# Performance work log

Measured on AMD Instinct MI355X. Metric: run time of the kernel, lower is better.

The kernel has to match this reference:

```python
import jax, jax.numpy as jnp
import numpy as np

EPS = 1e-6
H, KV, HD, FF = 16, 8, 128, 3072

def rmsnorm(x, scale):
    # qwen3_compatible: compute in fp32, scale, cast back
    xf = x.astype(jnp.float32)
    var = jnp.mean(xf * xf, axis=-1, keepdims=True)
    return ((xf * jax.lax.rsqrt(var + EPS)) * scale).astype(x.dtype)

def apply_rope(x, cos, sin):
    # x: [b, h, s, d]; cos/sin: [s, d]
    d = x.shape[-1]
    x1, x2 = x[..., : d // 2], x[..., d // 2 :]
    rotated = jnp.concatenate([-x2, x1], axis=-1)
    return (x * cos[None, None] + rotated * sin[None, None]).astype(x.dtype)

def setup_inputs() -> dict:
    key = jax.random.key(0)
    B, S, D = 2, 2048, 1024
    ks = jax.random.split(key, 8)
    x = jax.random.normal(ks[0], (B, S, D), jnp.float32)
    mask = jnp.triu(jnp.ones((S, S), dtype=bool), k=1)  # True = masked (causal)
    # Qwen3 RoPE, base 1e6, full-dim cos/sin (halves duplicated)
    pos = jnp.arange(S, dtype=jnp.float32)
    inv_freq = 1.0 / (1e6 ** (jnp.arange(0, HD, 2, dtype=jnp.float32) / HD))
    ang = pos[:, None] * inv_freq[None, :]
    cos = jnp.concatenate([jnp.cos(ang), jnp.cos(ang)], axis=-1)
    sin = jnp.concatenate([jnp.sin(ang), jnp.sin(ang)], axis=-1)
    s = 0.02
    wq = jax.random.normal(ks[1], (D, H * HD), jnp.float32) * s
    wk = jax.random.normal(ks[2], (D, KV * HD), jnp.float32) * s
    wv = jax.random.normal(ks[3], (D, KV * HD), jnp.float32) * s
    wo = jax.random.normal(ks[4], (H * HD, D), jnp.float32) * s
    fc1 = jax.random.normal(ks[5], (D, FF), jnp.float32) * s
    fc2 = jax.random.normal(ks[6], (D, FF), jnp.float32) * s
    fc3 = jax.random.normal(ks[7], (FF, D), jnp.float32) * s
    return dict(x=x, mask=mask, cos=cos, sin=sin, wq=wq, wk=wk, wv=wv, wo=wo,
                fc1=fc1, fc2=fc2, fc3=fc3,
                norm1_scale=jnp.ones((D,), jnp.float32),
                norm2_scale=jnp.ones((D,), jnp.float32),
                q_norm_scale=jnp.ones((HD,), jnp.float32),
                k_norm_scale=jnp.ones((HD,), jnp.float32))

def reference(x, mask, cos, sin, wq, wk, wv, wo, fc1, fc2, fc3,
              norm1_scale, norm2_scale, q_norm_scale, k_norm_scale):
    B, S, D = x.shape
    G = H // KV  # GQA group size
    # --- attention sublayer ---
    h = rmsnorm(x, norm1_scale)
    q = (h @ wq).reshape(B, S, H, HD).transpose(0, 2, 1, 3)   # [b,h,s,d]
    k = (h @ wk).reshape(B, S, KV, HD).transpose(0, 2, 1, 3)  # [b,kv,s,d]
    v = (h @ wv).reshape(B, S, KV, HD).transpose(0, 2, 1, 3)
    q = rmsnorm(q, q_norm_scale)
    k = rmsnorm(k, k_norm_scale)
    q = apply_rope(q, cos, sin)
    k = apply_rope(k, cos, sin)
    k = jnp.repeat(k, G, axis=1)  # repeat_interleave over head dim
    v = jnp.repeat(v, G, axis=1)
    scores = jnp.einsum('bhqd,bhkd->bhqk', q, k)
    scores = jnp.where(mask[None, None], -jnp.inf, scores)
    w = jax.nn.softmax(scores / np.float32(np.sqrt(HD)), axis=-1)
    ctx = jnp.einsum('bhqk,bhkd->bqhd', w, v).reshape(B, S, H * HD)
    x = x + ctx @ wo
    # --- SwiGLU FFN sublayer ---
    h2 = rmsnorm(x, norm2_scale)
    ff = (jax.nn.silu(h2 @ fc1) * (h2 @ fc2)) @ fc3
    return x + ff
```

## Files before the change

kernel.cpp:

```cpp
#include <hip/hip_runtime.h>

#define B_  2
#define S_  2048
#define D_  1024
#define H_  16
#define KV_ 8
#define HD_ 128
#define FF_ 3072
#define KVB 32

typedef short bf16x8 __attribute__((ext_vector_type(8)));
typedef short bf16x4 __attribute__((ext_vector_type(4)));
typedef float f32x4 __attribute__((ext_vector_type(4)));

__device__ __forceinline__ float bf2f(unsigned short u) {
    union { float f; unsigned int i; } c; c.i = ((unsigned int)u) << 16; return c.f;
}
__device__ __forceinline__ unsigned short f2bf(float f) {
    union { float f; unsigned int i; } c; c.f = f;
    unsigned int r = c.i + 0x7fffu + ((c.i >> 16) & 1u);
    return (unsigned short)(r >> 16);
}
__device__ __forceinline__ unsigned int cvtpk_bf16(float lo, float hi) {
    unsigned int r;
    asm("v_cvt_pk_bf16_f32 %0, %1, %2" : "=v"(r) : "v"(lo), "v"(hi));
    return r;
}

__device__ __forceinline__ void gload_lds16(const unsigned short* g, char* ldsbase) {
    __builtin_amdgcn_global_load_lds(
        (const __attribute__((address_space(1))) unsigned int*)g,
        (__attribute__((address_space(3))) unsigned int*)ldsbase, 16, 0, 0);
}

__device__ __forceinline__ f32x4 pv_mfma(bf16x4 a, bf16x4 b, f32x4 c) {
#if __has_builtin(__builtin_amdgcn_mfma_f32_16x16x16bf16_1k)
    return __builtin_amdgcn_mfma_f32_16x16x16bf16_1k(a, b, c, 0, 0, 0);
#elif __has_builtin(__builtin_amdgcn_mfma_f32_16x16x16_bf16)
    return __builtin_amdgcn_mfma_f32_16x16x16_bf16(a, b, c, 0, 0, 0);
#else
    f32x4 d;
    asm("v_mfma_f32_16x16x16_bf16 %0, %1, %2, %3" : "=v"(d) : "v"(a), "v"(b), "v"(c));
    return d;
#endif
}

__global__ __launch_bounds__(256)
void rmsnorm_kernel(const float* __restrict__ in, const float* __restrict__ scale,
                    unsigned short* __restrict__ out) {
    const int row = blockIdx.x;
    const int t = threadIdx.x;
    const float4 v = *reinterpret_cast<const float4*>(in + (size_t)row * D_ + t * 4);
    float s = v.x * v.x + v.y * v.y + v.z * v.z + v.w * v.w;
    #pragma unroll
    for (int o = 32; o; o >>= 1) s += __shfl_down(s, o);
    __shared__ float red[4];
    const int lane = t & 63, wid = t >> 6;
    if (lane == 0) red[wid] = s;
    __syncthreads();
    s = red[0] + red[1] + red[2] + red[3];
    const float rn = rsqrtf(s * (1.0f / D_) + 1e-6f);
    const float4 sc = *reinterpret_cast<const float4*>(scale + t * 4);
    unsigned short o4[4];
    o4[0] = f2bf(v.x * rn * sc.x);
    o4[1] = f2bf(v.y * rn * sc.y);
    o4[2] = f2bf(v.z * rn * sc.z);
    o4[3] = f2bf(v.w * rn * sc.w);
    *reinterpret_cast<ushort4*>(out + (size_t)row * D_ + t * 4) =
        *reinterpret_cast<ushort4*>(o4);
}

struct WTDesc {
    const float* src[7];
    unsigned short* dst[7];
    int K[7];
    int N[7];
    int start[8];
};

__global__ __launch_bounds__(256)
void wtrans_all_kernel(WTDesc d) {
    __shared__ float tile[32][33];
    const int blk = blockIdx.x;
    int i = 0;
    #pragma unroll
    for (int j = 0; j < 7; ++j) if (blk >= d.start[j + 1]) i = j + 1;
    const int local = blk - d.start[i];
    const int K = d.K[i], N = d.N[i];
    const int nkt = K >> 5;
    const int kt = (local % nkt) * 32, nt = (local / nkt) * 32;
    const float* W = d.src[i];
    unsigned short* Wt = d.dst[i];
    const int t = threadIdx.x;
    {
        const int r = t >> 3, c4 = (t & 7) * 4;
        const float4 v = *reinterpret_cast<const float4*>(W + (size_t)(kt + r) * N + nt + c4);
        tile[r][c4] = v.x; tile[r][c4 + 1] = v.y; tile[r][c4 + 2] = v.z; tile[r][c4 + 3] = v.w;
    }
    __syncthreads();
    {
        const int n = t >> 3, k4 = (t & 7) * 4;
        unsigned short o[4];
        #pragma unroll
        for (int q = 0; q < 4; q++) o[q] = f2bf(tile[k4 + q][n]);
        *reinterpret_cast<ushort4*>(Wt + (size_t)(nt + n) * K + kt + k4) =
            *reinterpret_cast<ushort4*>(o);
    }
}

__global__ __launch_bounds__(256)
void vtrans_kernel(const unsigned short* __restrict__ vin, unsigned short* __restrict__ vt) {
    __shared__ unsigned short tile[32][36];
    const int t = threadIdx.x;
    const int mt = blockIdx.x * 32, nt = blockIdx.y * 32;
    {
        const int r = t >> 3, c4 = (t & 7) * 4;
        *reinterpret_cast<ushort4*>(&tile[r][c4]) =
            *reinterpret_cast<const ushort4*>(vin + (size_t)(mt + r) * 4096 + nt + c4);
    }
    __syncthreads();
    {
        const int n = t >> 3, m4 = (t & 7) * 4;
        unsigned short o[4];
        #pragma unroll
        for (int q = 0; q < 4; q++) o[q] = tile[m4 + q][n];
        *reinterpret_cast<ushort4*>(vt + (size_t)(nt + n) * 4096 + mt + m4) =
            *reinterpret_cast<ushort4*>(o);
    }
}

__global__ __launch_bounds__(512, 2)
void gemm256(const unsigned short* __restrict__ A, const unsigned short* __restrict__ Bt,
             unsigned short* __restrict__ C, int M, int N, int K, int nm) {
    __shared__ __align__(16) char lds[131072];
    const int tid = threadIdx.x;
    const int lane = tid & 63, w = tid >> 6;
    const int lm = lane & 15, lg = lane >> 4;
    const int wr = w >> 2, wc = w & 3;
    const int nwg = gridDim.x;
    const int cpx = nwg >> 3;
    const int bid = blockIdx.x;
    const int swz = (bid & 7) * cpx + (bid >> 3);
    const int m0 = (swz % nm) * 256;
    const int n0 = (swz / nm) * 256;

    f32x4 acc[8][4];
    #pragma unroll
    for (int i = 0; i < 8; ++i)
        #pragma unroll
        for (int j = 0; j < 4; ++j) acc[i][j] = (f32x4){0.f, 0.f, 0.f, 0.f};

    const int srow = tid >> 3;
    const int skel = ((tid & 7) * 8) ^ (((tid >> 5) & 1) << 4);
    const int flip = ((lm >> 2) & 1) << 5;
    const int abase = (wr * 128 + lm) * 128 + ((lg * 16) ^ flip);
    const int bbase = (wc * 64 + lm) * 128 + ((lg * 16) ^ flip);

    auto part1 = [&](int kt, int d) {
        const unsigned short* ga = A + (size_t)(m0 + srow) * K + kt * 64 + skel;
        const unsigned short* gb = Bt + (size_t)(n0 + srow) * K + kt * 64 + skel;
        char* la = lds + d * 65536 + (w << 10);
        char* lb = la + 32768;
        gload_lds16(gb,                      lb);
        gload_lds16(gb + (size_t)64 * K,     lb + 8192);
        gload_lds16(gb + (size_t)128 * K,    lb + 16384);
        gload_lds16(gb + (size_t)192 * K,    lb + 24576);
        gload_lds16(ga,                      la);
        gload_lds16(ga + (size_t)128 * K,    la + 16384);
    };
    auto part2 = [&](int kt, int d) {
        const unsigned short* ga = A + (size_t)(m0 + srow) * K + kt * 64 + skel;
        char* la = lds + d * 65536 + (w << 10);
        gload_lds16(ga + (size_t)64 * K,     la + 8192);
        gload_lds16(ga + (size_t)192 * K,    la + 24576);
    };

    part1(0, 0);
    part2(0, 0);
    asm volatile("s_waitcnt vmcnt(0)" ::: "memory");
    __builtin_amdgcn_s_barrier();

    const int ntile = K >> 6;
    for (int kt = 0; kt < ntile; ++kt) {
        const int d = kt & 1;
        const bool pf = (kt + 1 < ntile);
        const char* Ar = lds + d * 65536;
        const char* Br = Ar + 32768;
        bf16x8 bb[4][2];
        #pragma unroll
        for (int nf = 0; nf < 4; ++nf)
            #pragma unroll
            for (int s = 0; s < 2; ++s)
                bb[nf][s] = *reinterpret_cast<const bf16x8*>(Br + bbase + nf * 2048 + s * 64);
        bf16x8 aH[4][2];
        #pragma unroll
        for (int f = 0; f < 4; ++f)
            #pragma unroll
            for (int s = 0; s < 2; ++s)
                aH[f][s] = *reinterpret_cast<const bf16x8*>(Ar + abase + f * 2048 + s * 64);
        if (pf) part1(kt + 1, d ^ 1);
        __builtin_amdgcn_s_setprio(1);
        #pragma unroll
        for (int f = 0; f < 4; ++f)
            #pragma unroll
            for (int nf = 0; nf < 4; ++nf)
                #pragma unroll
                for (int s = 0; s < 2; ++s)
                    acc[f][nf] = __builtin_amdgcn_mfma_f32_16x16x32_bf16(
                        aH[f][s], bb[nf][s], acc[f][nf], 0, 0, 0);
        __builtin_amdgcn_s_setprio(0);
        if (pf) asm volatile("s_waitcnt vmcnt(6)" ::: "memory");
        else    asm volatile("s_waitcnt vmcnt(0)" ::: "memory");
        __builtin_amdgcn_s_barrier();
        #pragma unroll
        for (int f = 0; f < 4; ++f)
            #pragma unroll
            for (int s = 0; s < 2; ++s)
                aH[f][s] = *reinterpret_cast<const bf16x8*>(Ar + abase + 8192 + f * 2048 + s * 64);
        if (pf) part2(kt + 1, d ^ 1);
        __builtin_amdgcn_s_setprio(1);
        #pragma unroll
        for (int f = 0; f < 4; ++f)
            #pragma unroll
            for (int nf = 0; nf < 4; ++nf)
                #pragma unroll
                for (int s = 0; s < 2; ++s)
                    acc[4 + f][nf] = __builtin_amdgcn_mfma_f32_16x16x32_bf16(
                        aH[f][s], bb[nf][s], acc[4 + f][nf], 0, 0, 0);
        __builtin_amdgcn_s_setprio(0);
        if (pf) {
            asm volatile("s_waitcnt vmcnt(2)" ::: "memory");
            __builtin_amdgcn_s_barrier();
        }
    }

    #pragma unroll
    for (int mf = 0; mf < 8; ++mf)
        #pragma unroll
        for (int nf = 0; nf < 4; ++nf)
            #pragma unroll
            for (int r = 0; r < 4; ++r)
                C[(size_t)(m0 + wr * 128 + mf * 16 + lg * 4 + r) * N +
                  (n0 + wc * 64 + nf * 16 + lm)] = f2bf(acc[mf][nf][r]);
}

template<int EPI>
__global__ __launch_bounds__(256)
void gemm_bt(const unsigned short* __restrict__ A, const unsigned short* __restrict__ Bt,
             void* __restrict__ Cout, const float* __restrict__ resid,
             int M, int N, int K, int lda) {
    __shared__ __align__(16) char sm[16384];
    const int t = threadIdx.x;
    const int lane = t & 63, w = t >> 6;
    const int m0 = blockIdx.x * 128, n0 = blockIdx.y * 128;
    const int wr = w >> 1, wc = w & 1;
    const int lm = lane & 15, lg = lane >> 4;

    f32x4 acc[4][4];
    #pragma unroll
    for (int i = 0; i < 4; i++)
        #pragma unroll
        for (int j = 0; j < 4; j++) acc[i][j] = (f32x4){0.f, 0.f, 0.f, 0.f};

    const int row0 = t >> 2, kseg = (t & 3) * 8;
    const unsigned short* Ab = A + (size_t)(m0 + row0) * lda + kseg;
    const unsigned short* Bb = Bt + (size_t)(n0 + row0) * K + kseg;
    const size_t rstepA = (size_t)64 * lda;
    const size_t rstepB = (size_t)64 * K;
    char* ldsA = sm + w * 1024;
    char* ldsB = sm + 8192 + w * 1024;

    for (int k0 = 0; k0 < K; k0 += 32) {
        gload_lds16(Ab + k0, ldsA);
        gload_lds16(Ab + rstepA + k0, ldsA + 4096);
        gload_lds16(Bb + k0, ldsB);
        gload_lds16(Bb + rstepB + k0, ldsB + 4096);
        __syncthreads();
        bf16x8 aF[4], bF[4];
        #pragma unroll
        for (int i = 0; i < 4; i++)
            aF[i] = *reinterpret_cast<const bf16x8*>(sm + (wr * 64 + i * 16 + lm) * 64 + lg * 16);
        #pragma unroll
        for (int j = 0; j < 4; j++)
            bF[j] = *reinterpret_cast<const bf16x8*>(sm + 8192 + (wc * 64 + j * 16 + lm) * 64 + lg * 16);
        #pragma unroll
        for (int i = 0; i < 4; i++)
            #pragma unroll
            for (int j = 0; j < 4; j++)
                acc[i][j] = __builtin_amdgcn_mfma_f32_16x16x32_bf16(aF[i], bF[j], acc[i][j], 0, 0, 0);
        __syncthreads();
    }

    #pragma unroll
    for (int i = 0; i < 4; i++) {
        #pragma unroll
        for (int j = 0; j < 4; j++) {
            #pragma unroll
            for (int r = 0; r < 4; r++) {
                const int row = m0 + wr * 64 + i * 16 + lg * 4 + r;
                const int col = n0 + wc * 64 + j * 16 + lm;
                const size_t idx = (size_t)row * N + col;
                if (EPI == 0) {
                    reinterpret_cast<unsigned short*>(Cout)[idx] = f2bf(acc[i][j][r]);
                } else {
                    reinterpret_cast<float*>(Cout)[idx] = resid[idx] + acc[i][j][r];
                }
            }
        }
    }
}

__global__ __launch_bounds__(128)
void qknorm_rope_kernel(unsigned short* __restrict__ qk, const float* __restrict__ scale,
                        const float* __restrict__ cosb, const float* __restrict__ sinb,
                        int ld, float oscale) {
    const int row = blockIdx.x;
    const int head = blockIdx.y;
    const int s = row & (S_ - 1);
    const int t = threadIdx.x;
    unsigned short* p = qk + (size_t)row * ld + head * HD_;
    const float v = bf2f(p[t]);
    float ss = v * v;
    #pragma unroll
    for (int o = 32; o; o >>= 1) ss += __shfl_down(ss, o);
    __shared__ float red[2];
    __shared__ float vals[HD_];
    const int lane = t & 63, wid = t >> 6;
    if (lane == 0) red[wid] = ss;
    __syncthreads();
    ss = red[0] + red[1];
    const float rn = rsqrtf(ss * (1.0f / HD_) + 1e-6f);
    const float nv = v * rn * scale[t];
    vals[t] = nv;
    __syncthreads();
    const float rot = (t < 64) ? -vals[t + 64] : vals[t - 64];
    const float c = cosb[(size_t)s * HD_ + t];
    const float sn = sinb[(size_t)s * HD_ + t];
    p[t] = f2bf((nv * c + rot * sn) * oscale);
}

__global__ __launch_bounds__(256)
void fattn_kernel(const unsigned short* __restrict__ qg,
                  const unsigned short* __restrict__ kg,
                  const unsigned short* __restrict__ vtg,
                  unsigned short* __restrict__ out, int qld, int kld) {
    __shared__ __align__(16) char klds[2 * 8192];
    __shared__ __align__(16) char vtlds[2 * 9216];
    const int t = threadIdx.x;
    const int lane = t & 63, w = t >> 6;
    const int lm = lane & 15, lg = lane >> 4;
    const int g = blockIdx.x;
    const int h = g & 15, b = g >> 4;
    const int qt = (int)gridDim.y - 1 - (int)blockIdx.y;
    const int kvh = h >> 1;
    const int q0b = qt * 64;
    const int q0w = q0b + w * 16;

    const unsigned short* qbase = qg + (size_t)(b * S_ + q0w + lm) * qld + h * HD_;
    bf16x8 qf[4];
    #pragma unroll
    for (int kk = 0; kk < 4; ++kk)
        qf[kk] = *reinterpret_cast<const bf16x8*>(qbase + kk * 32 + lg * 8);

    f32x4 acc[8];
    #pragma unroll
    for (int i = 0; i < 8; ++i) acc[i] = (f32x4){0.f, 0.f, 0.f, 0.f};
    float m = -3e38f, l = 0.f;

    const int nt = 2 * qt + 2;
    const int skv = t >> 3, sd8 = t & 7;
    const int vd = t >> 1, vseg = t & 1;
    const unsigned short* kgb = kg + (size_t)b * S_ * kld + kvh * HD_;
    const unsigned short* vgb = vtg + (size_t)(kvh * HD_) * (B_ * S_) + (size_t)b * S_;

    uint4 kr0, kr1, vr0, vr1;
    auto LOADR = [&](int kt) {
        const int kv0 = kt * KVB;
        const unsigned short* ksrc = kgb + (size_t)(kv0 + skv) * kld + sd8 * 16;
        kr0 = *reinterpret_cast<const uint4*>(ksrc);
        kr1 = *reinterpret_cast<const uint4*>(ksrc + 8);
        const unsigned short* vsrc = vgb + (size_t)vd * (B_ * S_) + kv0 + vseg * 16;
        vr0 = *reinterpret_cast<const uint4*>(vsrc);
        vr1 = *reinterpret_cast<const uint4*>(vsrc + 8);
    };
    auto WRITELDS = [&](int bufi) {
        char* kd = klds + bufi * 8192 + skv * 256;
        const int sw = (skv & 7) << 4;
        *reinterpret_cast<uint4*>(kd + ((sd8 * 32) ^ sw)) = kr0;
        *reinterpret_cast<uint4*>(kd + ((sd8 * 32 + 16) ^ sw)) = kr1;
        char* vdst = vtlds + bufi * 9216 + vd * 72 + vseg * 32;
        *reinterpret_cast<uint2*>(vdst)      = make_uint2(vr0.x, vr0.y);
        *reinterpret_cast<uint2*>(vdst + 8)  = make_uint2(vr0.z, vr0.w);
        *reinterpret_cast<uint2*>(vdst + 16) = make_uint2(vr1.x, vr1.y);
        *reinterpret_cast<uint2*>(vdst + 24) = make_uint2(vr1.z, vr1.w);
    };

    LOADR(0);
    WRITELDS(0);
    __syncthreads();

    for (int kt = 0; kt < nt; ++kt) {
        const int kv0 = kt * KVB;
        const int bufi = kt & 1;
        const bool havenext = (kt + 1 < nt);
        if (havenext) LOADR(kt + 1);
        if (kv0 <= q0w + 15) {
            f32x4 st[2];
            st[0] = (f32x4){0.f, 0.f, 0.f, 0.f};
            st[1] = (f32x4){0.f, 0.f, 0.f, 0.f};
            #pragma unroll
            for (int sub = 0; sub < 2; ++sub) {
                const int kvl = sub * 16 + lm;
                const char* krow = klds + bufi * 8192 + kvl * 256;
                const int sw = (kvl & 7) << 4;
                #pragma unroll
                for (int kk = 0; kk < 4; ++kk) {
                    const bf16x8 kf = *reinterpret_cast<const bf16x8*>(krow + ((kk * 64 + lg * 16) ^ sw));
                    st[sub] = __builtin_amdgcn_mfma_f32_16x16x32_bf16(kf, qf[kk], st[sub], 0, 0, 0);
                }
            }
            if (kv0 + KVB - 1 > q0w) {
                const int qa = q0w + lm;
                #pragma unroll
                for (int sub = 0; sub < 2; ++sub)
                    #pragma unroll
                    for (int r = 0; r < 4; ++r)
                        if (kv0 + sub * 16 + lg * 4 + r > qa) st[sub][r] = -3e38f;
            }
            float pmax = st[0][0];
            #pragma unroll
            for (int r = 1; r < 4; ++r) pmax = fmaxf(pmax, st[0][r]);
            #pragma unroll
            for (int r = 0; r < 4; ++r) pmax = fmaxf(pmax, st[1][r]);
            pmax = fmaxf(pmax, __shfl_xor(pmax, 16));
            pmax = fmaxf(pmax, __shfl_xor(pmax, 32));
            if (__any(pmax - m > 1.0f)) {
                const float mn = fmaxf(pmax, m);
                const float corr = exp2f(m - mn);
                l *= corr;
                #pragma unroll
                for (int i = 0; i < 8; ++i) acc[i] *= corr;
                m = mn;
            }
            float p[8];
            #pragma unroll
            for (int sub = 0; sub < 2; ++sub)
                #pragma unroll
                for (int r = 0; r < 4; ++r)
                    p[sub * 4 + r] = exp2f(st[sub][r] - m);
            float ps = (p[0] + p[1]) + (p[2] + p[3]) + (p[4] + p[5]) + (p[6] + p[7]);
            ps += __shfl_xor(ps, 16);
            ps += __shfl_xor(ps, 32);
            l += ps;
            bf16x4 pb[2];
            #pragma unroll
            for (int sub = 0; sub < 2; ++sub) {
                union { unsigned int u[2]; bf16x4 v; } pk;
                pk.u[0] = cvtpk_bf16(p[sub * 4 + 0], p[sub * 4 + 1]);
                pk.u[1] = cvtpk_bf16(p[sub * 4 + 2], p[sub * 4 + 3]);
                pb[sub] = pk.v;
            }
            #pragma unroll
            for (int sub = 0; sub < 2; ++sub) {
                const char* vb2 = vtlds + bufi * 9216 + sub * 32 + lg * 8;
                #pragma unroll
                for (int db = 0; db < 8; ++db) {
                    const bf16x4 vf = *reinterpret_cast<const bf16x4*>(vb2 + (db * 16 + lm) * 72);
                    acc[db] = pv_mfma(vf, pb[sub], acc[db]);
                }
            }
        }
        if (havenext) WRITELDS((kt + 1) & 1);
        __syncthreads();
    }
    const float inv = 1.0f / l;
    unsigned short* ob = out + (size_t)(b * S_ + q0w + lm) * qld + h * HD_ + lg * 4;
    #pragma unroll
    for (int db = 0; db < 8; ++db) {
        uint2 o2;
        o2.x = cvtpk_bf16(acc[db][0] * inv, acc[db][1] * inv);
        o2.y = cvtpk_bf16(acc[db][2] * inv, acc[db][3] * inv);
        *reinterpret_cast<uint2*>(ob + db * 16) = o2;
    }
}

__global__ __launch_bounds__(256)
void silu_mul_kernel(unsigned short* __restrict__ g, int n4) {
    const int i = blockIdx.x * 256 + threadIdx.x;
    if (i >= n4) return;
    const int r = i / (FF_ / 4);
    const int c = (i - r * (FF_ / 4)) * 4;
    const size_t off = (size_t)r * (2 * FF_) + c;
    const uint2 a = *reinterpret_cast<const uint2*>(g + off);
    const uint2 bv = *reinterpret_cast<const uint2*>(g + off + FF_);
    const unsigned int au[2] = {a.x, a.y}, bu[2] = {bv.x, bv.y};
    unsigned int rr[2];
    #pragma unroll
    for (int j = 0; j < 2; j++) {
        const float a0 = bf2f((unsigned short)(au[j] & 0xffff));
        const float a1 = bf2f((unsigned short)(au[j] >> 16));
        const float b0 = bf2f((unsigned short)(bu[j] & 0xffff));
        const float b1 = bf2f((unsigned short)(bu[j] >> 16));
        const float s0 = a0 / (1.f + __expf(-a0)) * b0;
        const float s1 = a1 / (1.f + __expf(-a1)) * b1;
        rr[j] = ((unsigned int)f2bf(s1) << 16) | (unsigned int)f2bf(s0);
    }
    *reinterpret_cast<uint2*>(g + off) = make_uint2(rr[0], rr[1]);
}

extern "C" void kernel_launch(void* const* d_in, const int* in_sizes, int n_in,
                              void* d_out, int out_size, void* d_ws, size_t ws_size,
                              hipStream_t stream) {
    const float* x    = (const float*)d_in[0];
    const float* cosb = (const float*)d_in[2];
    const float* sinb = (const float*)d_in[3];
    const float* wq   = (const float*)d_in[4];
    const float* wk   = (const float*)d_in[5];
    const float* wv   = (const float*)d_in[6];
    const float* wo   = (const float*)d_in[7];
    const float* fc1  = (const float*)d_in[8];
    const float* fc2  = (const float*)d_in[9];
    const float* fc3  = (const float*)d_in[10];
    const float* n1s  = (const float*)d_in[11];
    const float* n2s  = (const float*)d_in[12];
    const float* qns  = (const float*)d_in[13];
    const float* kns  = (const float*)d_in[14];

    char* ws = (char*)d_ws;
    const int M = B_ * S_;
    float* outf = (float*)d_out;
    const float CS = 0.12752409731504826f;

    unsigned short* h     = (unsigned short*)(ws);
    unsigned short* qkvb  = (unsigned short*)(ws + 8388608);
    unsigned short* vtb   = (unsigned short*)(ws + 41943040);
    unsigned short* g12   = (unsigned short*)(ws + 8388608);
    float*          x2    = (float*)(ws + 58720256);
    unsigned short* wqkvt = (unsigned short*)(ws + 75497472);
    unsigned short* wot   = (unsigned short*)(ws + 83886080);
    unsigned short* f12t  = (unsigned short*)(ws + 88080384);
    unsigned short* f3t   = (unsigned short*)(ws + 100663296);

    WTDesc wd;
    wd.src[0] = wq;  wd.dst[0] = wqkvt;                         wd.K[0] = D_;       wd.N[0] = 2048;
    wd.src[1] = wk;  wd.dst[1] = wqkvt + (size_t)2048 * 1024;   wd.K[1] = D_;       wd.N[1] = 1024;
    wd.src[2] = wv;  wd.dst[2] = wqkvt + (size_t)3072 * 1024;   wd.K[2] = D_;       wd.N[2] = 1024;
    wd.src[3] = wo;  wd.dst[3] = wot;                           wd.K[3] = H_ * HD_; wd.N[3] = D_;
    wd.src[4] = fc1; wd.dst[4] = f12t;                          wd.K[4] = D_;       wd.N[4] = FF_;
    wd.src[5] = fc2; wd.dst[5] = f12t + (size_t)3072 * 1024;    wd.K[5] = D_;       wd.N[5] = FF_;
    wd.src[6] = fc3; wd.dst[6] = f3t;                           wd.K[6] = FF_;      wd.N[6] = D_;
    wd.start[0] = 0;
    for (int i = 0; i < 7; ++i)
        wd.start[i + 1] = wd.start[i] + (wd.K[i] / 32) * (wd.N[i] / 32);
    wtrans_all_kernel<<<wd.start[7], 256, 0, stream>>>(wd);

    rmsnorm_kernel<<<M, 256, 0, stream>>>(x, n1s, h);
    gemm256<<<(M / 256) * (4096 / 256), 512, 0, stream>>>(h, wqkvt, qkvb, M, 4096, D_, M / 256);
    vtrans_kernel<<<dim3(M / 32, 1024 / 32), 256, 0, stream>>>(qkvb + 3072, vtb);
    qknorm_rope_kernel<<<dim3(M, H_), 128, 0, stream>>>(qkvb, qns, cosb, sinb, 4096, CS);
    qknorm_rope_kernel<<<dim3(M, KV_), 128, 0, stream>>>(qkvb + 2048, kns, cosb, sinb, 4096, 1.0f);
    fattn_kernel<<<dim3(H_ * B_, S_ / 64), 256, 0, stream>>>(qkvb, qkvb + 2048, vtb, qkvb, 4096, 4096);
    gemm_bt<1><<<dim3(M / 128, D_ / 128), 256, 0, stream>>>(qkvb, wot, x2, x, M, D_, H_ * HD_, 4096);
    rmsnorm_kernel<<<M, 256, 0, stream>>>(x2, n2s, h);
    gemm256<<<(M / 256) * (6144 / 256), 512, 0, stream>>>(h, f12t, g12, M, 6144, D_, M / 256);
    silu_mul_kernel<<<(M * FF_ / 4 + 255) / 256, 256, 0, stream>>>(g12, M * FF_ / 4);
    gemm_bt<1><<<dim3(M / 128, D_ / 128), 256, 0, stream>>>(g12, f3t, outf, x2, M, D_, FF_, 2 * FF_);
}
```

Measured before the change: 392.4 us.

## Switch flash attention to 32x32x16 MFMA with 128-query tiles

Flash attention now uses 32x32x16 bf16 MFMA instructions, so each wave handles 32 query rows and each block handles 128 queries, halving the number of blocks. The P matrix is repacked across half-waves with lane shuffles to match the operand layout of the larger MFMA. Each K/V tile loaded into LDS is reused by more queries and fewer, larger MFMA instructions are issued per tile. The cost is higher register pressure (a 64-float accumulator), fewer blocks, which worsens causal load imbalance, and extra cross-lane shuffles.

```diff
diff --git a/kernel.cpp b/kernel.cpp
--- a/kernel.cpp
+++ b/kernel.cpp
@@ -10,8 +10,8 @@
 #define KVB 32
 
 typedef short bf16x8 __attribute__((ext_vector_type(8)));
-typedef short bf16x4 __attribute__((ext_vector_type(4)));
 typedef float f32x4 __attribute__((ext_vector_type(4)));
+typedef float f32x16 __attribute__((ext_vector_type(16)));
 
 __device__ __forceinline__ float bf2f(unsigned short u) {
     union { float f; unsigned int i; } c; c.i = ((unsigned int)u) << 16; return c.f;
@@ -31,18 +31,6 @@
     __builtin_amdgcn_global_load_lds(
         (const __attribute__((address_space(1))) unsigned int*)g,
         (__attribute__((address_space(3))) unsigned int*)ldsbase, 16, 0, 0);
-}
-
-__device__ __forceinline__ f32x4 pv_mfma(bf16x4 a, bf16x4 b, f32x4 c) {
-#if __has_builtin(__builtin_amdgcn_mfma_f32_16x16x16bf16_1k)
-    return __builtin_amdgcn_mfma_f32_16x16x16bf16_1k(a, b, c, 0, 0, 0);
-#elif __has_builtin(__builtin_amdgcn_mfma_f32_16x16x16_bf16)
-    return __builtin_amdgcn_mfma_f32_16x16x16_bf16(a, b, c, 0, 0, 0);
-#else
-    f32x4 d;
-    asm("v_mfma_f32_16x16x16_bf16 %0, %1, %2, %3" : "=v"(d) : "v"(a), "v"(b), "v"(c));
-    return d;
-#endif
 }
 
 __global__ __launch_bounds__(256)
@@ -339,7 +327,7 @@
     p[t] = f2bf((nv * c + rot * sn) * oscale);
 }
 
-__global__ __launch_bounds__(256)
+__global__ __launch_bounds__(256, 2)
 void fattn_kernel(const unsigned short* __restrict__ qg,
                   const unsigned short* __restrict__ kg,
                   const unsigned short* __restrict__ vtg,
@@ -348,26 +336,28 @@
     __shared__ __align__(16) char vtlds[2 * 9216];
     const int t = threadIdx.x;
     const int lane = t & 63, w = t >> 6;
-    const int lm = lane & 15, lg = lane >> 4;
+    const int lq = lane & 31, lh = lane >> 5;
     const int g = blockIdx.x;
     const int h = g & 15, b = g >> 4;
     const int qt = (int)gridDim.y - 1 - (int)blockIdx.y;
     const int kvh = h >> 1;
-    const int q0b = qt * 64;
-    const int q0w = q0b + w * 16;
-
-    const unsigned short* qbase = qg + (size_t)(b * S_ + q0w + lm) * qld + h * HD_;
-    bf16x8 qf[4];
-    #pragma unroll
-    for (int kk = 0; kk < 4; ++kk)
-        qf[kk] = *reinterpret_cast<const bf16x8*>(qbase + kk * 32 + lg * 8);
-
-    f32x4 acc[8];
-    #pragma unroll
-    for (int i = 0; i < 8; ++i) acc[i] = (f32x4){0.f, 0.f, 0.f, 0.f};
+    const int q0b = qt * 128;
+    const int q0w = q0b + w * 32;
+
+    const unsigned short* qbase = qg + (size_t)(b * S_ + q0w + lq) * qld + h * HD_;
+    bf16x8 qf[8];
+    #pragma unroll
+    for (int kk = 0; kk < 8; ++kk)
+        qf[kk] = *reinterpret_cast<const bf16x8*>(qbase + kk * 16 + lh * 8);
+
+    f32x16 acc[4];
+    #pragma unroll
+    for (int i = 0; i < 4; ++i)
+        #pragma unroll
+        for (int r = 0; r < 16; ++r) acc[i][r] = 0.f;
     float m = -3e38f, l = 0.f;
 
-    const int nt = 2 * qt + 2;
+    const int nt = 4 * qt + 4;
     const int skv = t >> 3, sd8 = t & 7;
     const int vd = t >> 1, vseg = t & 1;
     const unsigned short* kgb = kg + (size_t)b * S_ * kld + kvh * HD_;
@@ -399,74 +389,78 @@
     WRITELDS(0);
     __syncthreads();
 
+    const int swr = (lq & 7) << 4;
+
     for (int kt = 0; kt < nt; ++kt) {
         const int kv0 = kt * KVB;
         const int bufi = kt & 1;
         const bool havenext = (kt + 1 < nt);
         if (havenext) LOADR(kt + 1);
-        if (kv0 <= q0w + 15) {
-            f32x4 st[2];
-            st[0] = (f32x4){0.f, 0.f, 0.f, 0.f};
-            st[1] = (f32x4){0.f, 0.f, 0.f, 0.f};
-            #pragma unroll
-            for (int sub = 0; sub < 2; ++sub) {
-                const int kvl = sub * 16 + lm;
-                const char* krow = klds + bufi * 8192 + kvl * 256;
-                const int sw = (kvl & 7) << 4;
-                #pragma unroll
-                for (int kk = 0; kk < 4; ++kk) {
-                    const bf16x8 kf = *reinterpret_cast<const bf16x8*>(krow + ((kk * 64 + lg * 16) ^ sw));
-                    st[sub] = __builtin_amdgcn_mfma_f32_16x16x32_bf16(kf, qf[kk], st[sub], 0, 0, 0);
-                }
+        if (kv0 <= q0w + 31) {
+            f32x16 st;
+            #pragma unroll
+            for (int r = 0; r < 16; ++r) st[r] = 0.f;
+            const char* krow = klds + bufi * 8192 + lq * 256;
+            #pragma unroll
+            for (int kk = 0; kk < 8; ++kk) {
+                const bf16x8 kf = *reinterpret_cast<const bf16x8*>(
+                    krow + ((kk * 32 + lh * 16) ^ swr));
+                st = __builtin_amdgcn_mfma_f32_32x32x16_bf16(kf, qf[kk], st, 0, 0, 0);
             }
             if (kv0 + KVB - 1 > q0w) {
-                const int qa = q0w + lm;
+                const int qa = q0w + lq;
                 #pragma unroll
-                for (int sub = 0; sub < 2; ++sub)
-                    #pragma unroll
-                    for (int r = 0; r < 4; ++r)
-                        if (kv0 + sub * 16 + lg * 4 + r > qa) st[sub][r] = -3e38f;
+                for (int r = 0; r < 16; ++r)
+                    if (kv0 + (r & 3) + 8 * (r >> 2) + 4 * lh > qa) st[r] = -3e38f;
             }
-            float pmax = st[0][0];
-            #pragma unroll
-            for (int r = 1; r < 4; ++r) pmax = fmaxf(pmax, st[0][r]);
-            #pragma unroll
-            for (int r = 0; r < 4; ++r) pmax = fmaxf(pmax, st[1][r]);
-            pmax = fmaxf(pmax, __shfl_xor(pmax, 16));
+            float pmax = st[0];
+            #pragma unroll
+            for (int r = 1; r < 16; ++r) pmax = fmaxf(pmax, st[r]);
             pmax = fmaxf(pmax, __shfl_xor(pmax, 32));
             if (__any(pmax - m > 1.0f)) {
                 const float mn = fmaxf(pmax, m);
                 const float corr = exp2f(m - mn);
                 l *= corr;
                 #pragma unroll
-                for (int i = 0; i < 8; ++i) acc[i] *= corr;
+                for (int i = 0; i < 4; ++i)
+                    #pragma unroll
+                    for (int r = 0; r < 16; ++r) acc[i][r] *= corr;
                 m = mn;
             }
-            float p[8];
-            #pragma unroll
-            for (int sub = 0; sub < 2; ++sub)
-                #pragma unroll
-                for (int r = 0; r < 4; ++r)
-                    p[sub * 4 + r] = exp2f(st[sub][r] - m);
-            float ps = (p[0] + p[1]) + (p[2] + p[3]) + (p[4] + p[5]) + (p[6] + p[7]);
-            ps += __shfl_xor(ps, 16);
+            float p[16];
+            #pragma unroll
+            for (int r = 0; r < 16; ++r) p[r] = exp2f(st[r] - m);
+            float ps = 0.f;
+            #pragma unroll
+            for (int r = 0; r < 16; ++r) ps += p[r];
             ps += __shfl_xor(ps, 32);
             l += ps;
-            bf16x4 pb[2];
-            #pragma unroll
-            for (int sub = 0; sub < 2; ++sub) {
-                union { unsigned int u[2]; bf16x4 v; } pk;
-                pk.u[0] = cvtpk_bf16(p[sub * 4 + 0], p[sub * 4 + 1]);
-                pk.u[1] = cvtpk_bf16(p[sub * 4 + 2], p[sub * 4 + 3]);
-                pb[sub] = pk.v;
+            bf16x8 pb[2];
+            #pragma unroll
+            for (int hh = 0; hh < 2; ++hh) {
+                const unsigned int c01 = cvtpk_bf16(p[hh * 8 + 0], p[hh * 8 + 1]);
+                const unsigned int c23 = cvtpk_bf16(p[hh * 8 + 2], p[hh * 8 + 3]);
+                const unsigned int c45 = cvtpk_bf16(p[hh * 8 + 4], p[hh * 8 + 5]);
+                const unsigned int c67 = cvtpk_bf16(p[hh * 8 + 6], p[hh * 8 + 7]);
+                const unsigned int x01 = (unsigned int)__shfl_xor((int)c01, 32);
+                const unsigned int x23 = (unsigned int)__shfl_xor((int)c23, 32);
+                const unsigned int x45 = (unsigned int)__shfl_xor((int)c45, 32);
+                const unsigned int x67 = (unsigned int)__shfl_xor((int)c67, 32);
+                union { unsigned int u[4]; bf16x8 v; } pk;
+                pk.u[0] = lh ? x45 : c01;
+                pk.u[1] = lh ? x67 : c23;
+                pk.u[2] = lh ? c45 : x01;
+                pk.u[3] = lh ? c67 : x23;
+                pb[hh] = pk.v;
             }
-            #pragma unroll
-            for (int sub = 0; sub < 2; ++sub) {
-                const char* vb2 = vtlds + bufi * 9216 + sub * 32 + lg * 8;
+            const char* vb2 = vtlds + bufi * 9216 + lh * 16;
+            #pragma unroll
+            for (int db = 0; db < 4; ++db) {
                 #pragma unroll
-                for (int db = 0; db < 8; ++db) {
-                    const bf16x4 vf = *reinterpret_cast<const bf16x4*>(vb2 + (db * 16 + lm) * 72);
-                    acc[db] = pv_mfma(vf, pb[sub], acc[db]);
+                for (int hh = 0; hh < 2; ++hh) {
+                    const bf16x8 vf = *reinterpret_cast<const bf16x8*>(
+                        vb2 + (db * 32 + lq) * 72 + hh * 32);
+                    acc[db] = __builtin_amdgcn_mfma_f32_32x32x16_bf16(vf, pb[hh], acc[db], 0, 0, 0);
                 }
             }
         }
@@ -474,13 +468,16 @@
         __syncthreads();
     }
     const float inv = 1.0f / l;
-    unsigned short* ob = out + (size_t)(b * S_ + q0w + lm) * qld + h * HD_ + lg * 4;
-    #pragma unroll
-    for (int db = 0; db < 8; ++db) {
-        uint2 o2;
-        o2.x = cvtpk_bf16(acc[db][0] * inv, acc[db][1] * inv);
-        o2.y = cvtpk_bf16(acc[db][2] * inv, acc[db][3] * inv);
-        *reinterpret_cast<uint2*>(ob + db * 16) = o2;
+    unsigned short* ob = out + (size_t)(b * S_ + q0w + lq) * qld + h * HD_;
+    #pragma unroll
+    for (int db = 0; db < 4; ++db) {
+        #pragma unroll
+        for (int gq = 0; gq < 4; ++gq) {
+            uint2 o2;
+            o2.x = cvtpk_bf16(acc[db][4 * gq + 0] * inv, acc[db][4 * gq + 1] * inv);
+            o2.y = cvtpk_bf16(acc[db][4 * gq + 2] * inv, acc[db][4 * gq + 3] * inv);
+            *reinterpret_cast<uint2*>(ob + db * 32 + 8 * gq + 4 * lh) = o2;
+        }
     }
 }
 
@@ -559,7 +556,7 @@
     vtrans_kernel<<<dim3(M / 32, 1024 / 32), 256, 0, stream>>>(qkvb + 3072, vtb);
     qknorm_rope_kernel<<<dim3(M, H_), 128, 0, stream>>>(qkvb, qns, cosb, sinb, 4096, CS);
     qknorm_rope_kernel<<<dim3(M, KV_), 128, 0, stream>>>(qkvb + 2048, kns, cosb, sinb, 4096, 1.0f);
-    fattn_kernel<<<dim3(H_ * B_, S_ / 64), 256, 0, stream>>>(qkvb, qkvb + 2048, vtb, qkvb, 4096, 4096);
+    fattn_kernel<<<dim3(H_ * B_, S_ / 128), 256, 0, stream>>>(qkvb, qkvb + 2048, vtb, qkvb, 4096, 4096);
     gemm_bt<1><<<dim3(M / 128, D_ / 128), 256, 0, stream>>>(qkvb, wot, x2, x, M, D_, H_ * HD_, 4096);
     rmsnorm_kernel<<<M, 256, 0, stream>>>(x2, n2s, h);
     gemm256<<<(M / 256) * (6144 / 256), 512, 0, stream>>>(h, f12t, g12, M, 6144, D_, M / 256);
```

Result: slower. 450.4 us (+14.8%).

## Fuse SiLU-gate multiply into FC1/FC2 GEMM epilogue via interleaved weight layout

Applied to the files above, without the earlier changes.

The fc1 and fc2 transposed weights are interleaved in 128-row blocks so that each 256-wide output tile of the gate GEMM holds matching gate and up columns. In the epilogue, the gate half is exchanged through LDS and the other waves compute silu(g1)*g2 and write a compact M x FF result. The separate silu_mul kernel and the round trip of the full 2*FF intermediate are removed, and the down projection now reads a dense buffer with lda=FF. This adds an LDS exchange and two barriers to the epilogue, and only half the waves do the final writes.

```diff
diff --git a/kernel.cpp b/kernel.cpp
--- a/kernel.cpp
+++ b/kernel.cpp
@@ -75,6 +75,7 @@
     unsigned short* dst[7];
     int K[7];
     int N[7];
+    int mode[7];
     int start[8];
 };
 
@@ -87,6 +88,7 @@
     for (int j = 0; j < 7; ++j) if (blk >= d.start[j + 1]) i = j + 1;
     const int local = blk - d.start[i];
     const int K = d.K[i], N = d.N[i];
+    const int mode = d.mode[i];
     const int nkt = K >> 5;
     const int kt = (local % nkt) * 32, nt = (local / nkt) * 32;
     const float* W = d.src[i];
@@ -100,10 +102,12 @@
     __syncthreads();
     {
         const int n = t >> 3, k4 = (t & 7) * 4;
+        int R = nt + n;
+        if (mode) R = (R >> 7) * 256 + ((mode == 2) ? 128 : 0) + (R & 127);
         unsigned short o[4];
         #pragma unroll
         for (int q = 0; q < 4; q++) o[q] = f2bf(tile[k4 + q][n]);
-        *reinterpret_cast<ushort4*>(Wt + (size_t)(nt + n) * K + kt + k4) =
+        *reinterpret_cast<ushort4*>(Wt + (size_t)R * K + kt + k4) =
             *reinterpret_cast<ushort4*>(o);
     }
 }
@@ -129,6 +133,7 @@
     }
 }
 
+template<int GLU>
 __global__ __launch_bounds__(512, 2)
 void gemm256(const unsigned short* __restrict__ A, const unsigned short* __restrict__ Bt,
              unsigned short* __restrict__ C, int M, int N, int K, int nm) {
@@ -234,14 +239,45 @@
         }
     }
 
-    #pragma unroll
-    for (int mf = 0; mf < 8; ++mf)
-        #pragma unroll
-        for (int nf = 0; nf < 4; ++nf)
-            #pragma unroll
-            for (int r = 0; r < 4; ++r)
-                C[(size_t)(m0 + wr * 128 + mf * 16 + lg * 4 + r) * N +
-                  (n0 + wc * 64 + nf * 16 + lm)] = f2bf(acc[mf][nf][r]);
+    if (GLU == 0) {
+        #pragma unroll
+        for (int mf = 0; mf < 8; ++mf)
+            #pragma unroll
+            for (int nf = 0; nf < 4; ++nf)
+                #pragma unroll
+                for (int r = 0; r < 4; ++r)
+                    C[(size_t)(m0 + wr * 128 + mf * 16 + lg * 4 + r) * N +
+                      (n0 + wc * 64 + nf * 16 + lm)] = f2bf(acc[mf][nf][r]);
+    } else {
+        __syncthreads();
+        float (*xch)[128] = reinterpret_cast<float(*)[128]>(lds);
+        if (wc < 2) {
+            #pragma unroll
+            for (int mf = 0; mf < 8; ++mf)
+                #pragma unroll
+                for (int nf = 0; nf < 4; ++nf)
+                    #pragma unroll
+                    for (int r = 0; r < 4; ++r)
+                        xch[wr * 128 + mf * 16 + lg * 4 + r][wc * 64 + nf * 16 + lm] =
+                            acc[mf][nf][r];
+        }
+        __syncthreads();
+        if (wc >= 2) {
+            const int nblk = swz / nm;
+            #pragma unroll
+            for (int mf = 0; mf < 8; ++mf)
+                #pragma unroll
+                for (int nf = 0; nf < 4; ++nf)
+                    #pragma unroll
+                    for (int r = 0; r < 4; ++r) {
+                        const int row = wr * 128 + mf * 16 + lg * 4 + r;
+                        const int col = (wc - 2) * 64 + nf * 16 + lm;
+                        const float g1 = xch[row][col];
+                        const float s = g1 / (1.f + __expf(-g1)) * acc[mf][nf][r];
+                        C[(size_t)(m0 + row) * FF_ + nblk * 128 + col] = f2bf(s);
+                    }
+        }
+    }
 }
 
 template<int EPI>
@@ -484,30 +520,6 @@
     }
 }
 
-__global__ __launch_bounds__(256)
-void silu_mul_kernel(unsigned short* __restrict__ g, int n4) {
-    const int i = blockIdx.x * 256 + threadIdx.x;
-    if (i >= n4) return;
-    const int r = i / (FF_ / 4);
-    const int c = (i - r * (FF_ / 4)) * 4;
-    const size_t off = (size_t)r * (2 * FF_) + c;
-    const uint2 a = *reinterpret_cast<const uint2*>(g + off);
-    const uint2 bv = *reinterpret_cast<const uint2*>(g + off + FF_);
-    const unsigned int au[2] = {a.x, a.y}, bu[2] = {bv.x, bv.y};
-    unsigned int rr[2];
-    #pragma unroll
-    for (int j = 0; j < 2; j++) {
-        const float a0 = bf2f((unsigned short)(au[j] & 0xffff));
-        const float a1 = bf2f((unsigned short)(au[j] >> 16));
-        const float b0 = bf2f((unsigned short)(bu[j] & 0xffff));
-        const float b1 = bf2f((unsigned short)(bu[j] >> 16));
-        const float s0 = a0 / (1.f + __expf(-a0)) * b0;
-        const float s1 = a1 / (1.f + __expf(-a1)) * b1;
-        rr[j] = ((unsigned int)f2bf(s1) << 16) | (unsigned int)f2bf(s0);
-    }
-    *reinterpret_cast<uint2*>(g + off) = make_uint2(rr[0], rr[1]);
-}
-
 extern "C" void kernel_launch(void* const* d_in, const int* in_sizes, int n_in,
                               void* d_out, int out_size, void* d_ws, size_t ws_size,
                               hipStream_t stream) {
@@ -534,35 +546,34 @@
     unsigned short* h     = (unsigned short*)(ws);
     unsigned short* qkvb  = (unsigned short*)(ws + 8388608);
     unsigned short* vtb   = (unsigned short*)(ws + 41943040);
-    unsigned short* g12   = (unsigned short*)(ws + 8388608);
+    unsigned short* gated = (unsigned short*)(ws + 8388608);
     float*          x2    = (float*)(ws + 58720256);
     unsigned short* wqkvt = (unsigned short*)(ws + 75497472);
     unsigned short* wot   = (unsigned short*)(ws + 83886080);
-    unsigned short* f12t  = (unsigned short*)(ws + 88080384);
+    unsigned short* f12g  = (unsigned short*)(ws + 88080384);
     unsigned short* f3t   = (unsigned short*)(ws + 100663296);
 
     WTDesc wd;
-    wd.src[0] = wq;  wd.dst[0] = wqkvt;                         wd.K[0] = D_;       wd.N[0] = 2048;
-    wd.src[1] = wk;  wd.dst[1] = wqkvt + (size_t)2048 * 1024;   wd.K[1] = D_;       wd.N[1] = 1024;
-    wd.src[2] = wv;  wd.dst[2] = wqkvt + (size_t)3072 * 1024;   wd.K[2] = D_;       wd.N[2] = 1024;
-    wd.src[3] = wo;  wd.dst[3] = wot;                           wd.K[3] = H_ * HD_; wd.N[3] = D_;
-    wd.src[4] = fc1; wd.dst[4] = f12t;                          wd.K[4] = D_;       wd.N[4] = FF_;
-    wd.src[5] = fc2; wd.dst[5] = f12t + (size_t)3072 * 1024;    wd.K[5] = D_;       wd.N[5] = FF_;
-    wd.src[6] = fc3; wd.dst[6] = f3t;                           wd.K[6] = FF_;      wd.N[6] = D_;
+    wd.src[0] = wq;  wd.dst[0] = wqkvt;                       wd.K[0] = D_;       wd.N[0] = 2048; wd.mode[0] = 0;
+    wd.src[1] = wk;  wd.dst[1] = wqkvt + (size_t)2048 * 1024; wd.K[1] = D_;       wd.N[1] = 1024; wd.mode[1] = 0;
+    wd.src[2] = wv;  wd.dst[2] = wqkvt + (size_t)3072 * 1024; wd.K[2] = D_;       wd.N[2] = 1024; wd.mode[2] = 0;
+    wd.src[3] = wo;  wd.dst[3] = wot;                         wd.K[3] = H_ * HD_; wd.N[3] = D_;   wd.mode[3] = 0;
+    wd.src[4] = fc1; wd.dst[4] = f12g;                        wd.K[4] = D_;       wd.N[4] = FF_;  wd.mode[4] = 1;
+    wd.src[5] = fc2; wd.dst[5] = f12g;                        wd.K[5] = D_;       wd.N[5] = FF_;  wd.mode[5] = 2;
+    wd.src[6] = fc3; wd.dst[6] = f3t;                         wd.K[6] = FF_;      wd.N[6] = D_;   wd.mode[6] = 0;
     wd.start[0] = 0;
     for (int i = 0; i < 7; ++i)
         wd.start[i + 1] = wd.start[i] + (wd.K[i] / 32) * (wd.N[i] / 32);
     wtrans_all_kernel<<<wd.start[7], 256, 0, stream>>>(wd);
 
     rmsnorm_kernel<<<M, 256, 0, stream>>>(x, n1s, h);
-    gemm256<<<(M / 256) * (4096 / 256), 512, 0, stream>>>(h, wqkvt, qkvb, M, 4096, D_, M / 256);
+    gemm256<0><<<(M / 256) * (4096 / 256), 512, 0, stream>>>(h, wqkvt, qkvb, M, 4096, D_, M / 256);
     vtrans_kernel<<<dim3(M / 32, 1024 / 32), 256, 0, stream>>>(qkvb + 3072, vtb);
     qknorm_rope_kernel<<<dim3(M, H_), 128, 0, stream>>>(qkvb, qns, cosb, sinb, 4096, CS);
     qknorm_rope_kernel<<<dim3(M, KV_), 128, 0, stream>>>(qkvb + 2048, kns, cosb, sinb, 4096, 1.0f);
     fattn_kernel<<<dim3(H_ * B_, S_ / 64), 256, 0, stream>>>(qkvb, qkvb + 2048, vtb, qkvb, 4096, 4096);
     gemm_bt<1><<<dim3(M / 128, D_ / 128), 256, 0, stream>>>(qkvb, wot, x2, x, M, D_, H_ * HD_, 4096);
     rmsnorm_kernel<<<M, 256, 0, stream>>>(x2, n2s, h);
-    gemm256<<<(M / 256) * (6144 / 256), 512, 0, stream>>>(h, f12t, g12, M, 6144, D_, M / 256);
-    silu_mul_kernel<<<(M * FF_ / 4 + 255) / 256, 256, 0, stream>>>(g12, M * FF_ / 4);
-    gemm_bt<1><<<dim3(M / 128, D_ / 128), 256, 0, stream>>>(g12, f3t, outf, x2, M, D_, FF_, 2 * FF_);
-}
+    gemm256<1><<<(M / 256) * (6144 / 256), 512, 0, stream>>>(h, f12g, gated, M, 6144, D_, M / 256);
+    gemm_bt<1><<<dim3(M / 128, D_ / 128), 256, 0, stream>>>(gated, f3t, outf, x2, M, D_, FF_, FF_);
+}
```

New measurement: 388.9 us. About the same (-0.9%).
